# Optimization experiments

Measured on AMD Instinct MI355X. Metric: run time of the kernel, lower is better.

Reference implementation:

```python
import jax, jax.numpy as jnp
import numpy as np

N_NODES = 50000
N_EDGES = 800000
IN_CH = 128
HID = 128
NUM_GRAPHS = 512
BN_EPS = 1e-5


def setup_inputs() -> dict:
    key = jax.random.key(0)
    ks = jax.random.split(key, 16)
    x = jax.random.normal(ks[0], (N_NODES, IN_CH), dtype=jnp.float32)
    edge_index = jax.random.randint(ks[1], (2, N_EDGES), 0, N_NODES, dtype=jnp.int64)
    batch = jnp.sort(jax.random.randint(ks[2], (N_NODES,), 0, NUM_GRAPHS, dtype=jnp.int64))

    def glorot(k, shape):
        fan_in = shape[1]
        return jax.random.normal(k, shape, dtype=jnp.float32) / jnp.sqrt(jnp.float32(fan_in))

    # SAGEConv1: lin_l (aggr path, with bias), lin_r (root path, no bias)
    W1l = glorot(ks[3], (HID, IN_CH)); b1 = jnp.zeros((HID,), jnp.float32)
    W1r = glorot(ks[4], (HID, IN_CH))
    # SAGEConv2
    W2l = glorot(ks[5], (HID, HID)); b2 = jnp.zeros((HID,), jnp.float32)
    W2r = glorot(ks[6], (HID, HID))
    # MLP tail
    lin1_w = glorot(ks[7], (HID, HID)); lin1_b = jnp.zeros((HID,), jnp.float32)
    lin2_w = glorot(ks[8], (2, HID)); lin2_b = jnp.zeros((2,), jnp.float32)
    # BatchNorm1d (eval mode, running stats)
    gamma = jnp.ones((HID,), jnp.float32)
    beta = jnp.zeros((HID,), jnp.float32)
    running_mean = jax.random.normal(ks[9], (HID,), dtype=jnp.float32) * 0.1
    running_var = jax.random.uniform(ks[10], (HID,), dtype=jnp.float32, minval=0.5, maxval=1.5)
    return {
        "x": x, "edge_index": edge_index, "batch": batch,
        "W1l": W1l, "b1": b1, "W1r": W1r,
        "W2l": W2l, "b2": b2, "W2r": W2r,
        "lin1_w": lin1_w, "lin1_b": lin1_b,
        "lin2_w": lin2_w, "lin2_b": lin2_b,
        "gamma": gamma, "beta": beta,
        "running_mean": running_mean, "running_var": running_var,
    }


def _sage_conv(x, src, dst, Wl, bl, Wr):
    # mean-aggregate neighbor features (message flows src -> dst)
    n = x.shape[0]
    agg = jax.ops.segment_sum(x[src], dst, num_segments=n)  # [N, d]
    cnt = jax.ops.segment_sum(jnp.ones((src.shape[0], 1), x.dtype), dst, num_segments=n)
    mean = agg / jnp.maximum(cnt, 1.0)
    return mean @ Wl.T + bl + x @ Wr.T


def reference(x, edge_index, batch, W1l, b1, W1r, W2l, b2, W2r,
              lin1_w, lin1_b, lin2_w, lin2_b, gamma, beta,
              running_mean, running_var):
    src, dst = edge_index[0], edge_index[1]
    h = _sage_conv(x, src, dst, W1l, b1, W1r)      # [N, HID]
    h = _sage_conv(h, src, dst, W2l, b2, W2r)      # [N, HID]
    h = jax.ops.segment_sum(h, batch, num_segments=NUM_GRAPHS)  # global_add_pool -> [G, HID]
    h = h @ lin1_w.T + lin1_b
    # BatchNorm1d in eval mode (running stats)
    h = (h - running_mean) * jax.lax.rsqrt(running_var + BN_EPS) * gamma + beta
    h = jax.nn.relu(h)
    h = h @ lin2_w.T + lin2_b                      # [G, 2]
    # Dropout is identity in eval mode
    return h
```

## Files before the change

### kernel.cpp

```cpp
#include <hip/hip_runtime.h>
#include <hip/hip_bf16.h>

#define NN 50000
#define NE 800000
#define HID 128
#define NG 512
#define BN_EPS 1e-5f

typedef __attribute__((ext_vector_type(8))) short bf16x8;
typedef __attribute__((ext_vector_type(4))) float f32x4;

__device__ __forceinline__ ushort f2bf(float f) {
    uint u = __float_as_uint(f);
    uint r = (u + 0x7fffu + ((u >> 16) & 1u)) >> 16;
    return (ushort)r;
}
__device__ __forceinline__ float bf_lo(uint v) { return __uint_as_float(v << 16); }
__device__ __forceinline__ float bf_hi(uint v) { return __uint_as_float(v & 0xffff0000u); }

#define NCH 64
#define CHE 12500
#define NRNG 4
#define HRNG 12500
#define HWORDS 6250
#define HIST_BLOCKS (NCH * NRNG)
#define CONV_BLOCKS 6250
#define WPREP_BLOCKS 32
#define POOLZ_BLOCKS 64
#define PH_GRID (HIST_BLOCKS + CONV_BLOCKS + WPREP_BLOCKS + POOLZ_BLOCKS)

__global__ __launch_bounds__(256) void prep_hist_kernel(const int* __restrict__ ei,
                                                        ushort* __restrict__ rank,
                                                        ushort* __restrict__ blockcnt,
                                                        const float* __restrict__ x,
                                                        ushort* __restrict__ xb,
                                                        const float* __restrict__ W0,
                                                        const float* __restrict__ W1,
                                                        const float* __restrict__ W2,
                                                        const float* __restrict__ W3,
                                                        ushort* __restrict__ Wp,
                                                        float* __restrict__ pooled) {
    __shared__ uint hh[HWORDS];
    uint b = blockIdx.x;
    if (b < HIST_BLOCKS) {
        int c = b >> 2;
        int r = b & 3;
        for (int i = threadIdx.x; i < HWORDS; i += 256) hh[i] = 0;
        __syncthreads();
        int base = c * CHE;
        int lo = r * HRNG;
        const int4* ev = (const int4*)(ei + NE + base);
        const int nvec = CHE / 4;
        int k4 = threadIdx.x;
        int4 cur;
        bool have = k4 < nvec;
        if (have) cur = ev[k4];
        while (have) {
            int kn = k4 + 256;
            bool hn = kn < nvec;
            int4 nxt;
            if (hn) nxt = ev[kn];
            int e0 = base + k4 * 4;
#pragma unroll
            for (int j = 0; j < 4; ++j) {
                int d = (j == 0) ? cur.x : (j == 1) ? cur.y : (j == 2) ? cur.z : cur.w;
                int local = d - lo;
                if ((unsigned)local < (unsigned)HRNG) {
                    uint sh = (local & 1) << 4;
                    uint old = atomicAdd(&hh[local >> 1], 1u << sh);
                    rank[e0 + j] = (ushort)((old >> sh) & 0xffffu);
                }
            }
            k4 = kn;
            cur = nxt;
            have = hn;
        }
        __syncthreads();
        uint* dstw = (uint*)(blockcnt + (size_t)c * NN) + r * HWORDS;
        for (int i = threadIdx.x; i < HWORDS; i += 256) dstw[i] = hh[i];
    } else if (b < HIST_BLOCKS + CONV_BLOCKS) {
        int i = (b - HIST_BLOCKS) * 256 + threadIdx.x;
        float4 v = ((const float4*)x)[i];
        ushort4 o;
        o.x = f2bf(v.x);
        o.y = f2bf(v.y);
        o.z = f2bf(v.z);
        o.w = f2bf(v.w);
        ((ushort4*)xb)[i] = o;
    } else if (b < HIST_BLOCKS + CONV_BLOCKS + WPREP_BLOCKS) {
        int wu = (b - HIST_BLOCKS - CONV_BLOCKS) * 4 + (threadIdx.x >> 6);
        if (wu >= 128) return;
        int lane = threadIdx.x & 63;
        int m = wu >> 5;
        int g = wu & 31;
        int tile = g >> 2;
        int chunk = g & 3;
        const float* W = (m == 0) ? W0 : (m == 1) ? W1 : (m == 2) ? W2 : W3;
        int col = tile * 16 + (lane & 15);
        int k0 = chunk * 32 + (lane >> 4) * 8;
        ushort* dst = Wp + ((size_t)wu * 64 + lane) * 8;
#pragma unroll
        for (int j = 0; j < 8; ++j) dst[j] = f2bf(W[col * HID + k0 + j]);
    } else {
        int i = (b - HIST_BLOCKS - CONV_BLOCKS - WPREP_BLOCKS) * 256 + threadIdx.x;
        ((float4*)pooled)[i] = make_float4(0.f, 0.f, 0.f, 0.f);
    }
}

__global__ __launch_bounds__(256) void scan1_kernel(ushort* __restrict__ blockcnt,
                                                    int* __restrict__ deg,
                                                    int* __restrict__ row_start,
                                                    int* __restrict__ bsums, int n) {
    __shared__ int wsum[4];
    __shared__ int degsh[256];
    int i = blockIdx.x * 256 + threadIdx.x;
    int w = blockIdx.x * 128 + (int)threadIdx.x;
    if (threadIdx.x < 128 && w < NN / 2) {
        uint run_lo = 0, run_hi = 0;
        uint* col = (uint*)blockcnt + w;
#pragma unroll 4
        for (int c = 0; c < NCH; ++c) {
            uint x = col[(size_t)c * (NN / 2)];
            col[(size_t)c * (NN / 2)] = run_lo | (run_hi << 16);
            run_lo += x & 0xffffu;
            run_hi += x >> 16;
        }
        degsh[2 * (int)threadIdx.x] = (int)run_lo;
        degsh[2 * (int)threadIdx.x + 1] = (int)run_hi;
        ((int2*)deg)[w] = make_int2((int)run_lo, (int)run_hi);
    }
    __syncthreads();
    int lane = threadIdx.x & 63;
    int wid = threadIdx.x >> 6;
    int v = (i < n) ? degsh[threadIdx.x] : 0;
    int sc = v;
#pragma unroll
    for (int off = 1; off < 64; off <<= 1) {
        int t = __shfl_up(sc, off);
        if (lane >= off) sc += t;
    }
    if (lane == 63) wsum[wid] = sc;
    __syncthreads();
    int wpre = 0;
#pragma unroll
    for (int k = 0; k < 4; ++k) wpre += (k < wid) ? wsum[k] : 0;
    if (i < n) row_start[i] = wpre + sc - v;
    if (threadIdx.x == 255) bsums[blockIdx.x] = wpre + sc;
}

__global__ __launch_bounds__(256) void scan23_kernel(int* __restrict__ row_start,
                                                     const int* __restrict__ bsums, int n) {
    __shared__ int sred[4];
    int v = (threadIdx.x < blockIdx.x) ? bsums[threadIdx.x] : 0;
#pragma unroll
    for (int off = 32; off > 0; off >>= 1) v += __shfl_xor(v, off);
    if ((threadIdx.x & 63) == 0) sred[threadIdx.x >> 6] = v;
    __syncthreads();
    int total = sred[0] + sred[1] + sred[2] + sred[3];
    int i = blockIdx.x * 256 + threadIdx.x;
    if (i < n) row_start[i] += total;
}

__global__ __launch_bounds__(256) void fill_kernel(const int* __restrict__ ei,
                                                   const int* __restrict__ row_start,
                                                   const ushort* __restrict__ rank,
                                                   const ushort* __restrict__ blockcnt,
                                                   ushort* __restrict__ srclist) {
    int e4 = blockIdx.x * 256 + threadIdx.x;
    if (e4 >= NE / 4) return;
    int4 src = ((const int4*)ei)[e4];
    int4 dst = ((const int4*)(ei + NE))[e4];
    ushort4 rk = ((const ushort4*)rank)[e4];
    int c = e4 / (CHE / 4);
    const ushort* off = blockcnt + (size_t)c * NN;
    int p0 = row_start[dst.x] + off[dst.x] + rk.x;
    int p1 = row_start[dst.y] + off[dst.y] + rk.y;
    int p2 = row_start[dst.z] + off[dst.z] + rk.z;
    int p3 = row_start[dst.w] + off[dst.w] + rk.w;
    srclist[p0] = (ushort)src.x;
    srclist[p1] = (ushort)src.y;
    srclist[p2] = (ushort)src.z;
    srclist[p3] = (ushort)src.w;
}

__global__ __launch_bounds__(256) void aggregate_kernel(const ushort* __restrict__ feat,
                                                        const int* __restrict__ row_start,
                                                        const int* __restrict__ deg,
                                                        const ushort* __restrict__ srclist,
                                                        ushort* __restrict__ mean, int n) {
    int node = blockIdx.x * 4 + (threadIdx.x >> 6);
    if (node >= n) return;
    int lane = threadIdx.x & 63;
    int cl = lane & 15;
    int sub = lane >> 4;
    const uint4* fb = (const uint4*)feat;
    int s0 = row_start[node];
    int d = deg[node];

    float a[8];
#pragma unroll
    for (int i = 0; i < 8; ++i) a[i] = 0.f;

    int j = 0;
    for (; j + 16 <= d; j += 16) {
        int i0 = srclist[s0 + j + sub];
        int i1 = srclist[s0 + j + 4 + sub];
        int i2 = srclist[s0 + j + 8 + sub];
        int i3 = srclist[s0 + j + 12 + sub];
        uint4 v0 = fb[(size_t)i0 * 16 + cl];
        uint4 v1 = fb[(size_t)i1 * 16 + cl];
        uint4 v2 = fb[(size_t)i2 * 16 + cl];
        uint4 v3 = fb[(size_t)i3 * 16 + cl];
        a[0] += (bf_lo(v0.x) + bf_lo(v1.x)) + (bf_lo(v2.x) + bf_lo(v3.x));
        a[1] += (bf_hi(v0.x) + bf_hi(v1.x)) + (bf_hi(v2.x) + bf_hi(v3.x));
        a[2] += (bf_lo(v0.y) + bf_lo(v1.y)) + (bf_lo(v2.y) + bf_lo(v3.y));
        a[3] += (bf_hi(v0.y) + bf_hi(v1.y)) + (bf_hi(v2.y) + bf_hi(v3.y));
        a[4] += (bf_lo(v0.z) + bf_lo(v1.z)) + (bf_lo(v2.z) + bf_lo(v3.z));
        a[5] += (bf_hi(v0.z) + bf_hi(v1.z)) + (bf_hi(v2.z) + bf_hi(v3.z));
        a[6] += (bf_lo(v0.w) + bf_lo(v1.w)) + (bf_lo(v2.w) + bf_lo(v3.w));
        a[7] += (bf_hi(v0.w) + bf_hi(v1.w)) + (bf_hi(v2.w) + bf_hi(v3.w));
    }
    if (j < d) {
        int dm1 = d - 1;
        int k0 = j + sub;
        int k1 = j + 4 + sub;
        int k2 = j + 8 + sub;
        int k3 = j + 12 + sub;
        int i0 = srclist[s0 + min(k0, dm1)];
        int i1 = srclist[s0 + min(k1, dm1)];
        int i2 = srclist[s0 + min(k2, dm1)];
        int i3 = srclist[s0 + min(k3, dm1)];
        uint4 v0 = make_uint4(0u, 0u, 0u, 0u);
        uint4 v1 = make_uint4(0u, 0u, 0u, 0u);
        uint4 v2 = make_uint4(0u, 0u, 0u, 0u);
        uint4 v3 = make_uint4(0u, 0u, 0u, 0u);
        if (k0 < d) v0 = fb[(size_t)i0 * 16 + cl];
        if (k1 < d) v1 = fb[(size_t)i1 * 16 + cl];
        if (k2 < d) v2 = fb[(size_t)i2 * 16 + cl];
        if (k3 < d) v3 = fb[(size_t)i3 * 16 + cl];
        a[0] += (bf_lo(v0.x) + bf_lo(v1.x)) + (bf_lo(v2.x) + bf_lo(v3.x));
        a[1] += (bf_hi(v0.x) + bf_hi(v1.x)) + (bf_hi(v2.x) + bf_hi(v3.x));
        a[2] += (bf_lo(v0.y) + bf_lo(v1.y)) + (bf_lo(v2.y) + bf_lo(v3.y));
        a[3] += (bf_hi(v0.y) + bf_hi(v1.y)) + (bf_hi(v2.y) + bf_hi(v3.y));
        a[4] += (bf_lo(v0.z) + bf_lo(v1.z)) + (bf_lo(v2.z) + bf_lo(v3.z));
        a[5] += (bf_hi(v0.z) + bf_hi(v1.z)) + (bf_hi(v2.z) + bf_hi(v3.z));
        a[6] += (bf_lo(v0.w) + bf_lo(v1.w)) + (bf_lo(v2.w) + bf_lo(v3.w));
        a[7] += (bf_hi(v0.w) + bf_hi(v1.w)) + (bf_hi(v2.w) + bf_hi(v3.w));
    }

#pragma unroll
    for (int i = 0; i < 8; ++i) {
        float v = a[i];
        v += __shfl_xor(v, 16);
        v += __shfl_xor(v, 32);
        a[i] = v;
    }

    if (sub == 0) {
        float inv = 1.0f / fmaxf((float)d, 1.0f);
        uint4 o;
        o.x = (uint)f2bf(a[0] * inv) | ((uint)f2bf(a[1] * inv) << 16);
        o.y = (uint)f2bf(a[2] * inv) | ((uint)f2bf(a[3] * inv) << 16);
        o.z = (uint)f2bf(a[4] * inv) | ((uint)f2bf(a[5] * inv) << 16);
        o.w = (uint)f2bf(a[6] * inv) | ((uint)f2bf(a[7] * inv) << 16);
        ((uint4*)mean)[(size_t)node * 16 + cl] = o;
    }
}

template <bool POOL>
__global__ __launch_bounds__(256) void sage_gemm_mfma(const ushort* __restrict__ Amean,
                                                      const ushort* __restrict__ Aroot,
                                                      const ushort* __restrict__ WpL,
                                                      const float* __restrict__ bias,
                                                      const int* __restrict__ batch,
                                                      void* __restrict__ outv, int nwaves) {
    int w = blockIdx.x * 4 + (threadIdx.x >> 6);
    if (w >= nwaves) return;
    int lane = threadIdx.x & 63;
    int mrow = lane & 15;
    int quad = lane >> 4;
    int r0 = w * 16;

    f32x4 acc[8];
#pragma unroll
    for (int t = 0; t < 8; ++t) acc[t] = (f32x4){0.f, 0.f, 0.f, 0.f};

    const ushort* arow_m = Amean + ((size_t)(r0 + mrow)) * HID + quad * 8;
    const ushort* arow_r = Aroot + ((size_t)(r0 + mrow)) * HID + quad * 8;

#pragma unroll
    for (int half = 0; half < 2; ++half) {
        const ushort* arow = half ? arow_r : arow_m;
        const ushort* wb = WpL + (size_t)half * 16384 + (size_t)lane * 8;
#pragma unroll
        for (int c = 0; c < 4; ++c) {
            bf16x8 a = *(const bf16x8*)(arow + c * 32);
#pragma unroll
            for (int t = 0; t < 8; ++t) {
                bf16x8 b = *(const bf16x8*)(wb + (size_t)(t * 4 + c) * 512);
                acc[t] = __builtin_amdgcn_mfma_f32_16x16x32_bf16(a, b, acc[t], 0, 0, 0);
            }
        }
    }

    if (POOL) {
        float* pooled = (float*)outv;
        int rbase = r0 + quad * 4;
        int g0 = batch[rbase + 0];
        int g1 = batch[rbase + 1];
        int g2 = batch[rbase + 2];
        int g3 = batch[rbase + 3];
#pragma unroll
        for (int t = 0; t < 8; ++t) {
            int col = t * 16 + mrow;
            float bv = bias[col];
            float v0 = acc[t][0] + bv;
            float v1 = acc[t][1] + bv;
            float v2 = acc[t][2] + bv;
            float v3 = acc[t][3] + bv;
            int cg = g0;
            float s = v0;
            if (g1 == cg) s += v1; else { atomicAdd(&pooled[(size_t)cg * HID + col], s); cg = g1; s = v1; }
            if (g2 == cg) s += v2; else { atomicAdd(&pooled[(size_t)cg * HID + col], s); cg = g2; s = v2; }
            if (g3 == cg) s += v3; else { atomicAdd(&pooled[(size_t)cg * HID + col], s); cg = g3; s = v3; }
            atomicAdd(&pooled[(size_t)cg * HID + col], s);
        }
    } else {
        ushort* out = (ushort*)outv;
#pragma unroll
        for (int t = 0; t < 8; ++t) {
            int col = t * 16 + mrow;
            float bv = bias[col];
#pragma unroll
            for (int r = 0; r < 4; ++r) {
                int row = r0 + quad * 4 + r;
                out[(size_t)row * HID + col] = f2bf(acc[t][r] + bv);
            }
        }
    }
}

__global__ __launch_bounds__(128) void tail_kernel(const float* __restrict__ pooled,
                                                   const float* __restrict__ lin1_w,
                                                   const float* __restrict__ lin1_b,
                                                   const float* __restrict__ lin2_w,
                                                   const float* __restrict__ lin2_b,
                                                   const float* __restrict__ gamma,
                                                   const float* __restrict__ beta,
                                                   const float* __restrict__ rmean,
                                                   const float* __restrict__ rvar,
                                                   float* __restrict__ out) {
    __shared__ float Wt[64 * 128];
    __shared__ float p[128];
    __shared__ float tbuf[128];
    int g = blockIdx.x;
    int c = threadIdx.x;
    p[c] = pooled[g * HID + c];
    float acc = lin1_b[c];
    int kk = c & 63;
    int chalf = c >> 6;
    for (int k0 = 0; k0 < 128; k0 += 64) {
        __syncthreads();
        for (int i = 0; i < 64; ++i) {
            int crow = i * 2 + chalf;
            float v = lin1_w[crow * HID + k0 + kk];
            Wt[kk * 128 + (crow ^ (kk & 31))] = v;
        }
        __syncthreads();
#pragma unroll
        for (int k = 0; k < 64; ++k) {
            acc += p[k0 + k] * Wt[k * 128 + (c ^ (k & 31))];
        }
    }
    float v = (acc - rmean[c]) * rsqrtf(rvar[c] + BN_EPS) * gamma[c] + beta[c];
    v = fmaxf(v, 0.f);
    tbuf[c] = v;
    __syncthreads();
    int j = c >> 6;
    int lane = c & 63;
    float partial = tbuf[lane] * lin2_w[j * HID + lane] +
                    tbuf[lane + 64] * lin2_w[j * HID + lane + 64];
    for (int off = 32; off > 0; off >>= 1) partial += __shfl_down(partial, off);
    if (lane == 0) out[g * 2 + j] = partial + lin2_b[j];
}

extern "C" void kernel_launch(void* const* d_in, const int* in_sizes, int n_in,
                              void* d_out, int out_size, void* d_ws, size_t ws_size,
                              hipStream_t stream) {
    const float* x = (const float*)d_in[0];
    const int* ei = (const int*)d_in[1];
    const int* batch = (const int*)d_in[2];
    const float* W1l = (const float*)d_in[3];
    const float* b1 = (const float*)d_in[4];
    const float* W1r = (const float*)d_in[5];
    const float* W2l = (const float*)d_in[6];
    const float* b2 = (const float*)d_in[7];
    const float* W2r = (const float*)d_in[8];
    const float* lin1_w = (const float*)d_in[9];
    const float* lin1_b = (const float*)d_in[10];
    const float* lin2_w = (const float*)d_in[11];
    const float* lin2_b = (const float*)d_in[12];
    const float* gamma = (const float*)d_in[13];
    const float* beta = (const float*)d_in[14];
    const float* rmean = (const float*)d_in[15];
    const float* rvar = (const float*)d_in[16];
    float* out = (float*)d_out;

    const int N = NN, E = NE;
    const int NWAVES = N / 16;

    char* p = (char*)d_ws;
    auto carve = [&](size_t bytes) {
        void* r = (void*)p;
        p += (bytes + 255) & ~(size_t)255;
        return r;
    };
    int* deg = (int*)carve((size_t)N * 4);
    int* row_start = (int*)carve((size_t)N * 4);
    int* bsums = (int*)carve(1024 * 4);
    ushort* rank = (ushort*)carve((size_t)E * 2);
    ushort* blockcnt = (ushort*)carve((size_t)NCH * NN * 2);
    ushort* srclist = (ushort*)carve((size_t)E * 2 + 64);
    ushort* xb = (ushort*)carve((size_t)N * HID * 2);
    ushort* meanb = (ushort*)carve((size_t)N * HID * 2);
    ushort* h1 = (ushort*)carve((size_t)N * HID * 2);
    float* pooled = (float*)carve((size_t)NG * HID * 4);
    ushort* Wp = (ushort*)carve(4 * 32 * 64 * 8 * 2);

    prep_hist_kernel<<<PH_GRID, 256, 0, stream>>>(ei, rank, blockcnt, x, xb,
                                                  W1l, W1r, W2l, W2r, Wp, pooled);

    const int scanBlocks = (N + 255) / 256;
    scan1_kernel<<<scanBlocks, 256, 0, stream>>>(blockcnt, deg, row_start, bsums, N);
    scan23_kernel<<<scanBlocks, 256, 0, stream>>>(row_start, bsums, N);
    fill_kernel<<<(E / 4 + 255) / 256, 256, 0, stream>>>(ei, row_start, rank, blockcnt, srclist);

    aggregate_kernel<<<(N + 3) / 4, 256, 0, stream>>>(xb, row_start, deg, srclist, meanb, N);
    sage_gemm_mfma<false><<<(NWAVES + 3) / 4, 256, 0, stream>>>(meanb, xb, Wp, b1, nullptr, h1,
                                                                NWAVES);
    aggregate_kernel<<<(N + 3) / 4, 256, 0, stream>>>(h1, row_start, deg, srclist, meanb, N);
    sage_gemm_mfma<true><<<(NWAVES + 3) / 4, 256, 0, stream>>>(meanb, h1, Wp + 32768, b2, batch,
                                                               pooled, NWAVES);
    tail_kernel<<<NG, 128, 0, stream>>>(pooled, lin1_w, lin1_b, lin2_w, lin2_b,
                                        gamma, beta, rmean, rvar, out);
}
```

Before: 244.2 us.

## Fuse neighbor mean aggregation with SAGE MFMA GEMM via shared-memory tile

New measurement: 239.7 us. About the same (-1.8%).

```diff
diff --git a/kernel.cpp b/kernel.cpp
--- a/kernel.cpp
+++ b/kernel.cpp
@@ -183,141 +183,144 @@
     srclist[p3] = (ushort)src.w;
 }
 
-__global__ __launch_bounds__(256) void aggregate_kernel(const ushort* __restrict__ feat,
-                                                        const int* __restrict__ row_start,
-                                                        const int* __restrict__ deg,
-                                                        const ushort* __restrict__ srclist,
-                                                        ushort* __restrict__ mean, int n) {
-    int node = blockIdx.x * 4 + (threadIdx.x >> 6);
-    if (node >= n) return;
+template <bool POOL>
+__global__ __launch_bounds__(256) void sage_fused(const ushort* __restrict__ feat,
+                                                  const int* __restrict__ row_start,
+                                                  const int* __restrict__ deg,
+                                                  const ushort* __restrict__ srclist,
+                                                  const ushort* __restrict__ WpL,
+                                                  const float* __restrict__ bias,
+                                                  const int* __restrict__ batch,
+                                                  void* __restrict__ outv) {
+    __shared__ ushort As[16][136];
     int lane = threadIdx.x & 63;
+    int wv = threadIdx.x >> 6;
+    int base = blockIdx.x * 16;
     int cl = lane & 15;
     int sub = lane >> 4;
     const uint4* fb = (const uint4*)feat;
-    int s0 = row_start[node];
-    int d = deg[node];
-
-    float a[8];
-#pragma unroll
-    for (int i = 0; i < 8; ++i) a[i] = 0.f;
-
-    int j = 0;
-    for (; j + 16 <= d; j += 16) {
-        int i0 = srclist[s0 + j + sub];
-        int i1 = srclist[s0 + j + 4 + sub];
-        int i2 = srclist[s0 + j + 8 + sub];
-        int i3 = srclist[s0 + j + 12 + sub];
-        uint4 v0 = fb[(size_t)i0 * 16 + cl];
-        uint4 v1 = fb[(size_t)i1 * 16 + cl];
-        uint4 v2 = fb[(size_t)i2 * 16 + cl];
-        uint4 v3 = fb[(size_t)i3 * 16 + cl];
-        a[0] += (bf_lo(v0.x) + bf_lo(v1.x)) + (bf_lo(v2.x) + bf_lo(v3.x));
-        a[1] += (bf_hi(v0.x) + bf_hi(v1.x)) + (bf_hi(v2.x) + bf_hi(v3.x));
-        a[2] += (bf_lo(v0.y) + bf_lo(v1.y)) + (bf_lo(v2.y) + bf_lo(v3.y));
-        a[3] += (bf_hi(v0.y) + bf_hi(v1.y)) + (bf_hi(v2.y) + bf_hi(v3.y));
-        a[4] += (bf_lo(v0.z) + bf_lo(v1.z)) + (bf_lo(v2.z) + bf_lo(v3.z));
-        a[5] += (bf_hi(v0.z) + bf_hi(v1.z)) + (bf_hi(v2.z) + bf_hi(v3.z));
-        a[6] += (bf_lo(v0.w) + bf_lo(v1.w)) + (bf_lo(v2.w) + bf_lo(v3.w));
-        a[7] += (bf_hi(v0.w) + bf_hi(v1.w)) + (bf_hi(v2.w) + bf_hi(v3.w));
-    }
-    if (j < d) {
-        int dm1 = d - 1;
-        int k0 = j + sub;
-        int k1 = j + 4 + sub;
-        int k2 = j + 8 + sub;
-        int k3 = j + 12 + sub;
-        int i0 = srclist[s0 + min(k0, dm1)];
-        int i1 = srclist[s0 + min(k1, dm1)];
-        int i2 = srclist[s0 + min(k2, dm1)];
-        int i3 = srclist[s0 + min(k3, dm1)];
-        uint4 v0 = make_uint4(0u, 0u, 0u, 0u);
-        uint4 v1 = make_uint4(0u, 0u, 0u, 0u);
-        uint4 v2 = make_uint4(0u, 0u, 0u, 0u);
-        uint4 v3 = make_uint4(0u, 0u, 0u, 0u);
-        if (k0 < d) v0 = fb[(size_t)i0 * 16 + cl];
-        if (k1 < d) v1 = fb[(size_t)i1 * 16 + cl];
-        if (k2 < d) v2 = fb[(size_t)i2 * 16 + cl];
-        if (k3 < d) v3 = fb[(size_t)i3 * 16 + cl];
-        a[0] += (bf_lo(v0.x) + bf_lo(v1.x)) + (bf_lo(v2.x) + bf_lo(v3.x));
-        a[1] += (bf_hi(v0.x) + bf_hi(v1.x)) + (bf_hi(v2.x) + bf_hi(v3.x));
-        a[2] += (bf_lo(v0.y) + bf_lo(v1.y)) + (bf_lo(v2.y) + bf_lo(v3.y));
-        a[3] += (bf_hi(v0.y) + bf_hi(v1.y)) + (bf_hi(v2.y) + bf_hi(v3.y));
-        a[4] += (bf_lo(v0.z) + bf_lo(v1.z)) + (bf_lo(v2.z) + bf_lo(v3.z));
-        a[5] += (bf_hi(v0.z) + bf_hi(v1.z)) + (bf_hi(v2.z) + bf_hi(v3.z));
-        a[6] += (bf_lo(v0.w) + bf_lo(v1.w)) + (bf_lo(v2.w) + bf_lo(v3.w));
-        a[7] += (bf_hi(v0.w) + bf_hi(v1.w)) + (bf_hi(v2.w) + bf_hi(v3.w));
-    }
-
-#pragma unroll
-    for (int i = 0; i < 8; ++i) {
-        float v = a[i];
-        v += __shfl_xor(v, 16);
-        v += __shfl_xor(v, 32);
-        a[i] = v;
-    }
-
-    if (sub == 0) {
-        float inv = 1.0f / fmaxf((float)d, 1.0f);
-        uint4 o;
-        o.x = (uint)f2bf(a[0] * inv) | ((uint)f2bf(a[1] * inv) << 16);
-        o.y = (uint)f2bf(a[2] * inv) | ((uint)f2bf(a[3] * inv) << 16);
-        o.z = (uint)f2bf(a[4] * inv) | ((uint)f2bf(a[5] * inv) << 16);
-        o.w = (uint)f2bf(a[6] * inv) | ((uint)f2bf(a[7] * inv) << 16);
-        ((uint4*)mean)[(size_t)node * 16 + cl] = o;
-    }
-}
-
-template <bool POOL>
-__global__ __launch_bounds__(256) void sage_gemm_mfma(const ushort* __restrict__ Amean,
-                                                      const ushort* __restrict__ Aroot,
-                                                      const ushort* __restrict__ WpL,
-                                                      const float* __restrict__ bias,
-                                                      const int* __restrict__ batch,
-                                                      void* __restrict__ outv, int nwaves) {
-    int w = blockIdx.x * 4 + (threadIdx.x >> 6);
-    if (w >= nwaves) return;
-    int lane = threadIdx.x & 63;
+
+#pragma unroll 1
+    for (int i = 0; i < 4; ++i) {
+        int node = base + wv * 4 + i;
+        int s0 = row_start[node];
+        int d = deg[node];
+
+        float a[8];
+#pragma unroll
+        for (int k = 0; k < 8; ++k) a[k] = 0.f;
+
+        int j = 0;
+        for (; j + 16 <= d; j += 16) {
+            int i0 = srclist[s0 + j + sub];
+            int i1 = srclist[s0 + j + 4 + sub];
+            int i2 = srclist[s0 + j + 8 + sub];
+            int i3 = srclist[s0 + j + 12 + sub];
+            uint4 v0 = fb[(size_t)i0 * 16 + cl];
+            uint4 v1 = fb[(size_t)i1 * 16 + cl];
+            uint4 v2 = fb[(size_t)i2 * 16 + cl];
+            uint4 v3 = fb[(size_t)i3 * 16 + cl];
+            a[0] += (bf_lo(v0.x) + bf_lo(v1.x)) + (bf_lo(v2.x) + bf_lo(v3.x));
+            a[1] += (bf_hi(v0.x) + bf_hi(v1.x)) + (bf_hi(v2.x) + bf_hi(v3.x));
+            a[2] += (bf_lo(v0.y) + bf_lo(v1.y)) + (bf_lo(v2.y) + bf_lo(v3.y));
+            a[3] += (bf_hi(v0.y) + bf_hi(v1.y)) + (bf_hi(v2.y) + bf_hi(v3.y));
+            a[4] += (bf_lo(v0.z) + bf_lo(v1.z)) + (bf_lo(v2.z) + bf_lo(v3.z));
+            a[5] += (bf_hi(v0.z) + bf_hi(v1.z)) + (bf_hi(v2.z) + bf_hi(v3.z));
+            a[6] += (bf_lo(v0.w) + bf_lo(v1.w)) + (bf_lo(v2.w) + bf_lo(v3.w));
+            a[7] += (bf_hi(v0.w) + bf_hi(v1.w)) + (bf_hi(v2.w) + bf_hi(v3.w));
+        }
+        if (j < d) {
+            int dm1 = d - 1;
+            int k0 = j + sub;
+            int k1 = j + 4 + sub;
+            int k2 = j + 8 + sub;
+            int k3 = j + 12 + sub;
+            int i0 = srclist[s0 + min(k0, dm1)];
+            int i1 = srclist[s0 + min(k1, dm1)];
+            int i2 = srclist[s0 + min(k2, dm1)];
+            int i3 = srclist[s0 + min(k3, dm1)];
+            uint4 v0 = make_uint4(0u, 0u, 0u, 0u);
+            uint4 v1 = make_uint4(0u, 0u, 0u, 0u);
+            uint4 v2 = make_uint4(0u, 0u, 0u, 0u);
+            uint4 v3 = make_uint4(0u, 0u, 0u, 0u);
+            if (k0 < d) v0 = fb[(size_t)i0 * 16 + cl];
+            if (k1 < d) v1 = fb[(size_t)i1 * 16 + cl];
+            if (k2 < d) v2 = fb[(size_t)i2 * 16 + cl];
+            if (k3 < d) v3 = fb[(size_t)i3 * 16 + cl];
+            a[0] += (bf_lo(v0.x) + bf_lo(v1.x)) + (bf_lo(v2.x) + bf_lo(v3.x));
+            a[1] += (bf_hi(v0.x) + bf_hi(v1.x)) + (bf_hi(v2.x) + bf_hi(v3.x));
+            a[2] += (bf_lo(v0.y) + bf_lo(v1.y)) + (bf_lo(v2.y) + bf_lo(v3.y));
+            a[3] += (bf_hi(v0.y) + bf_hi(v1.y)) + (bf_hi(v2.y) + bf_hi(v3.y));
+            a[4] += (bf_lo(v0.z) + bf_lo(v1.z)) + (bf_lo(v2.z) + bf_lo(v3.z));
+            a[5] += (bf_hi(v0.z) + bf_hi(v1.z)) + (bf_hi(v2.z) + bf_hi(v3.z));
+            a[6] += (bf_lo(v0.w) + bf_lo(v1.w)) + (bf_lo(v2.w) + bf_lo(v3.w));
+            a[7] += (bf_hi(v0.w) + bf_hi(v1.w)) + (bf_hi(v2.w) + bf_hi(v3.w));
+        }
+
+#pragma unroll
+        for (int k = 0; k < 8; ++k) {
+            float v = a[k];
+            v += __shfl_xor(v, 16);
+            v += __shfl_xor(v, 32);
+            a[k] = v;
+        }
+
+        if (sub == 0) {
+            float inv = 1.0f / fmaxf((float)d, 1.0f);
+            uint4 o;
+            o.x = (uint)f2bf(a[0] * inv) | ((uint)f2bf(a[1] * inv) << 16);
+            o.y = (uint)f2bf(a[2] * inv) | ((uint)f2bf(a[3] * inv) << 16);
+            o.z = (uint)f2bf(a[4] * inv) | ((uint)f2bf(a[5] * inv) << 16);
+            o.w = (uint)f2bf(a[6] * inv) | ((uint)f2bf(a[7] * inv) << 16);
+            *(uint4*)&As[wv * 4 + i][cl * 8] = o;
+        }
+    }
+    __syncthreads();
+
     int mrow = lane & 15;
     int quad = lane >> 4;
-    int r0 = w * 16;
-
-    f32x4 acc[8];
-#pragma unroll
-    for (int t = 0; t < 8; ++t) acc[t] = (f32x4){0.f, 0.f, 0.f, 0.f};
-
-    const ushort* arow_m = Amean + ((size_t)(r0 + mrow)) * HID + quad * 8;
-    const ushort* arow_r = Aroot + ((size_t)(r0 + mrow)) * HID + quad * 8;
+
+    f32x4 acc[2];
+    acc[0] = (f32x4){0.f, 0.f, 0.f, 0.f};
+    acc[1] = (f32x4){0.f, 0.f, 0.f, 0.f};
+
+    const ushort* arow_r = feat + ((size_t)(base + mrow)) * HID + quad * 8;
 
 #pragma unroll
     for (int half = 0; half < 2; ++half) {
-        const ushort* arow = half ? arow_r : arow_m;
         const ushort* wb = WpL + (size_t)half * 16384 + (size_t)lane * 8;
 #pragma unroll
         for (int c = 0; c < 4; ++c) {
-            bf16x8 a = *(const bf16x8*)(arow + c * 32);
-#pragma unroll
-            for (int t = 0; t < 8; ++t) {
+            bf16x8 a;
+            if (half == 0) {
+                a = *(const bf16x8*)&As[mrow][c * 32 + quad * 8];
+            } else {
+                a = *(const bf16x8*)(arow_r + c * 32);
+            }
+#pragma unroll
+            for (int tt = 0; tt < 2; ++tt) {
+                int t = wv * 2 + tt;
                 bf16x8 b = *(const bf16x8*)(wb + (size_t)(t * 4 + c) * 512);
-                acc[t] = __builtin_amdgcn_mfma_f32_16x16x32_bf16(a, b, acc[t], 0, 0, 0);
+                acc[tt] = __builtin_amdgcn_mfma_f32_16x16x32_bf16(a, b, acc[tt], 0, 0, 0);
             }
         }
     }
 
     if (POOL) {
         float* pooled = (float*)outv;
-        int rbase = r0 + quad * 4;
+        int rbase = base + quad * 4;
         int g0 = batch[rbase + 0];
         int g1 = batch[rbase + 1];
         int g2 = batch[rbase + 2];
         int g3 = batch[rbase + 3];
 #pragma unroll
-        for (int t = 0; t < 8; ++t) {
-            int col = t * 16 + mrow;
+        for (int tt = 0; tt < 2; ++tt) {
+            int col = (wv * 2 + tt) * 16 + mrow;
             float bv = bias[col];
-            float v0 = acc[t][0] + bv;
-            float v1 = acc[t][1] + bv;
-            float v2 = acc[t][2] + bv;
-            float v3 = acc[t][3] + bv;
+            float v0 = acc[tt][0] + bv;
+            float v1 = acc[tt][1] + bv;
+            float v2 = acc[tt][2] + bv;
+            float v3 = acc[tt][3] + bv;
             int cg = g0;
             float s = v0;
             if (g1 == cg) s += v1; else { atomicAdd(&pooled[(size_t)cg * HID + col], s); cg = g1; s = v1; }
@@ -328,13 +331,13 @@
     } else {
         ushort* out = (ushort*)outv;
 #pragma unroll
-        for (int t = 0; t < 8; ++t) {
-            int col = t * 16 + mrow;
+        for (int tt = 0; tt < 2; ++tt) {
+            int col = (wv * 2 + tt) * 16 + mrow;
             float bv = bias[col];
 #pragma unroll
             for (int r = 0; r < 4; ++r) {
-                int row = r0 + quad * 4 + r;
-                out[(size_t)row * HID + col] = f2bf(acc[t][r] + bv);
+                int row = base + quad * 4 + r;
+                out[(size_t)row * HID + col] = f2bf(acc[tt][r] + bv);
             }
         }
     }
@@ -407,7 +410,6 @@
     float* out = (float*)d_out;
 
     const int N = NN, E = NE;
-    const int NWAVES = N / 16;
 
     char* p = (char*)d_ws;
     auto carve = [&](size_t bytes) {
@@ -422,7 +424,6 @@
     ushort* blockcnt = (ushort*)carve((size_t)NCH * NN * 2);
     ushort* srclist = (ushort*)carve((size_t)E * 2 + 64);
     ushort* xb = (ushort*)carve((size_t)N * HID * 2);
-    ushort* meanb = (ushort*)carve((size_t)N * HID * 2);
     ushort* h1 = (ushort*)carve((size_t)N * HID * 2);
     float* pooled = (float*)carve((size_t)NG * HID * 4);
     ushort* Wp = (ushort*)carve(4 * 32 * 64 * 8 * 2);
@@ -435,12 +436,10 @@
     scan23_kernel<<<scanBlocks, 256, 0, stream>>>(row_start, bsums, N);
     fill_kernel<<<(E / 4 + 255) / 256, 256, 0, stream>>>(ei, row_start, rank, blockcnt, srclist);
 
-    aggregate_kernel<<<(N + 3) / 4, 256, 0, stream>>>(xb, row_start, deg, srclist, meanb, N);
-    sage_gemm_mfma<false><<<(NWAVES + 3) / 4, 256, 0, stream>>>(meanb, xb, Wp, b1, nullptr, h1,
-                                                                NWAVES);
-    aggregate_kernel<<<(N + 3) / 4, 256, 0, stream>>>(h1, row_start, deg, srclist, meanb, N);
-    sage_gemm_mfma<true><<<(NWAVES + 3) / 4, 256, 0, stream>>>(meanb, h1, Wp + 32768, b2, batch,
-                                                               pooled, NWAVES);
+    sage_fused<false><<<N / 16, 256, 0, stream>>>(xb, row_start, deg, srclist, Wp, b1,
+                                                  nullptr, h1);
+    sage_fused<true><<<N / 16, 256, 0, stream>>>(h1, row_start, deg, srclist, Wp + 32768, b2,
+                                                 batch, pooled);
     tail_kernel<<<NG, 128, 0, stream>>>(pooled, lin1_w, lin1_b, lin2_w, lin2_b,
                                         gamma, beta, rmean, rvar, out);
 }
```
